# Kernel optimization log

Measured on AMD Instinct MI355X. Metric: run time of the kernel, lower is better.

Reference implementation:

```python
import jax, jax.numpy as jnp
import numpy as np

V, P, D, H, HD, L, FF = 21128, 512, 768, 12, 64, 12, 3072
COEF = np.array([[1,1,0,0,0,0,0,0,0,0,0,1],[1,1,1,1,0,0,0,0,0,0,0,1],[1,1,1,1,1,1,0,0,0,0,0,1],[1,1,1,1,1,1,1,1,0,0,0,1],[1,1,1,1,1,1,1,1,1,1,0,1]], dtype=np.float32)

def _ln(x, g, b):
    mu = jnp.mean(x, -1, keepdims=True)
    v = jnp.mean((x - mu) ** 2, -1, keepdims=True)
    return (x - mu) / jnp.sqrt(v + 1e-12) * g + b

def _gelu(x):
    return x * 0.5 * (1.0 + jax.lax.erf(x * 0.7071067811865475))

def setup_inputs() -> dict:
    key = jax.random.key(0)
    ks = jax.random.split(key, 16)
    B, S, LE = 16, 512, 256
    input_ids = jax.random.randint(ks[0], (B, S), 0, V)
    mask = jnp.ones((B, S), jnp.float32)
    epid = jax.random.randint(ks[1], (B, LE), 0, 10)
    epid = epid.at[:, -1].set(9)  # ensure encoder_turn=9 -> coefficient row 4
    s = 0.02
    def nrm(k, shape):
        return jax.random.normal(k, shape, jnp.float32) * s
    return {
        'input_ids': input_ids, 'mask': mask, 'encoder_position_id': epid,
        'word_emb': nrm(ks[2], (V, D)), 'pos_emb': nrm(ks[3], (P, D)),
        'emb_ln_g': jnp.ones((D,)), 'emb_ln_b': jnp.zeros((D,)),
        'Wq': nrm(ks[4], (L, D, D)), 'bq': jnp.zeros((L, D)),
        'Wk': nrm(ks[5], (L, D, D)), 'bk': jnp.zeros((L, D)),
        'Wv': nrm(ks[6], (L, D, D)), 'bv': jnp.zeros((L, D)),
        'Wo': nrm(ks[7], (L, D, D)), 'bo': jnp.zeros((L, D)),
        'ln1_g': jnp.ones((L, D)), 'ln1_b': jnp.zeros((L, D)),
        'Wi': nrm(ks[8], (L, D, FF)), 'bi': jnp.zeros((L, FF)),
        'Wo2': nrm(ks[9], (L, FF, D)), 'bo2': jnp.zeros((L, D)),
        'ln2_g': jnp.ones((L, D)), 'ln2_b': jnp.zeros((L, D)),
        'coef': jnp.tile(jnp.asarray(COEF)[None], (L, 1, 1)),
    }

def reference(input_ids, mask, encoder_position_id, word_emb, pos_emb, emb_ln_g, emb_ln_b,
              Wq, bq, Wk, bk, Wv, bv, Wo, bo, ln1_g, ln1_b, Wi, bi, Wo2, bo2, ln2_g, ln2_b, coef):
    B, S = input_ids.shape
    LE = encoder_position_id.shape[1]
    # causal+padding mask: floor((m+m^T)/2) on {0,1} == AND == product, then tril
    am = jnp.tril(mask[:, None, None, :] * mask[:, None, :, None])  # [B,1,S,S]
    # position coefficient machinery
    turn = jnp.max(encoder_position_id, -1)           # [B]
    row = ((turn - 1) // 2).astype(jnp.int32)         # row into [5,12] table
    enc_pm = jax.nn.one_hot(encoder_position_id, 12, dtype=jnp.float32)  # [B,LE,12]
    dec_pm = jnp.zeros((B, S - LE, 12), jnp.float32).at[:, :, 11].set(1.0)
    pm = jnp.concatenate([enc_pm, dec_pm], 1)         # [B,S,12]
    # embeddings (token_type not used in forward; past_length=0)
    h = _ln(word_emb[input_ids] + pos_emb[jnp.arange(S)], emb_ln_g, emb_ln_b)
    for l in range(L):
        coef_row = coef[l][row]                       # [B,12]
        ps = jnp.einsum('bsk,bk->bs', pm, coef_row)   # per-key modulation [B,S]
        q = (h @ Wq[l] + bq[l]).reshape(B, S, H, HD)
        k = (h @ Wk[l] + bk[l]).reshape(B, S, H, HD)
        v = (h @ Wv[l] + bv[l]).reshape(B, S, H, HD)
        scores = jnp.einsum('bqhd,bkhd->bhqk', q, k) / 8.0
        scores = scores * ps[:, None, None, :]
        scores = scores * am - 1e10 * (1.0 - am)
        probs = jax.nn.softmax(scores, -1)
        ctx = jnp.einsum('bhqk,bkhd->bqhd', probs, v).reshape(B, S, D)
        a = _ln(ctx @ Wo[l] + bo[l] + h, ln1_g[l], ln1_b[l])
        ff = _gelu(a @ Wi[l] + bi[l])
        h = _ln(ff @ Wo2[l] + bo2[l] + a, ln2_g[l], ln2_b[l])
    return h
```

## Files before the change

kernel.cpp:

```cpp
#include <hip/hip_runtime.h>

#define SEQ 512
#define NB  16
#define DIM 768
#define NH  12
#define HDIM 64
#define NL  12
#define FFD 3072
#define MTOK 8192
#define QKVD 2304

typedef _Float16 half8 __attribute__((ext_vector_type(8)));
typedef float    floatx4 __attribute__((ext_vector_type(4)));

__device__ __forceinline__ void load_lds16(const void* g, void* l) {
  __builtin_amdgcn_global_load_lds((__attribute__((address_space(1))) void*)g,
                                   (__attribute__((address_space(3))) void*)l, 16, 0, 0);
}

__device__ __forceinline__ float blockSum768(float v) {
  __shared__ float red[4];
  #pragma unroll
  for (int d = 32; d; d >>= 1) v += __shfl_xor(v, d);
  const int wv = threadIdx.x >> 6;
  __syncthreads();
  if ((threadIdx.x & 63) == 0) red[wv] = v;
  __syncthreads();
  return red[0] + red[1] + red[2] + red[3];
}

__device__ __forceinline__ void ln_store(float x0, float x1, float x2,
                                         const float* __restrict__ g,
                                         const float* __restrict__ bb,
                                         float* __restrict__ yf,
                                         _Float16* __restrict__ yh, int row) {
  const int tid = threadIdx.x;
  const float mu = blockSum768(x0 + x1 + x2) * (1.0f / 768.0f);
  const float d0 = x0 - mu, d1 = x1 - mu, d2 = x2 - mu;
  const float var = blockSum768(d0 * d0 + d1 * d1 + d2 * d2) * (1.0f / 768.0f);
  const float inv = rsqrtf(var + 1e-12f);
  const size_t base = (size_t)row * DIM;
  const float y0 = d0 * inv * g[tid]       + bb[tid];
  const float y1 = d1 * inv * g[tid + 256] + bb[tid + 256];
  const float y2 = d2 * inv * g[tid + 512] + bb[tid + 512];
  if (yf) { yf[base + tid] = y0; yf[base + tid + 256] = y1; yf[base + tid + 512] = y2; }
  yh[base + tid] = (_Float16)y0; yh[base + tid + 256] = (_Float16)y1; yh[base + tid + 512] = (_Float16)y2;
}

__global__ __launch_bounds__(256) void embed_ln_k(const int* __restrict__ ids,
                                                  const float* __restrict__ we,
                                                  const float* __restrict__ pe,
                                                  const float* __restrict__ g,
                                                  const float* __restrict__ bb,
                                                  float* __restrict__ hf,
                                                  _Float16* __restrict__ hh) {
  const int tok = blockIdx.x;
  const int s = tok & (SEQ - 1);
  const int id = ids[tok];
  const int tid = threadIdx.x;
  float x[3];
  #pragma unroll
  for (int j = 0; j < 3; ++j) {
    const int d = tid + j * 256;
    x[j] = we[(size_t)id * DIM + d] + pe[(size_t)s * DIM + d];
  }
  ln_store(x[0], x[1], x[2], g, bb, hf, hh, tok);
}

__global__ __launch_bounds__(256) void ln_k(const float* __restrict__ xin,
                                            const float* __restrict__ g,
                                            const float* __restrict__ bb,
                                            float* __restrict__ yf,
                                            _Float16* __restrict__ yh) {
  const int row = blockIdx.x;
  const int tid = threadIdx.x;
  float x[3];
  #pragma unroll
  for (int j = 0; j < 3; ++j) x[j] = xin[(size_t)row * DIM + tid + j * 256];
  ln_store(x[0], x[1], x[2], g, bb, yf, yh, row);
}

__global__ __launch_bounds__(256) void transpose_k(const float* __restrict__ in,
                                                   _Float16* __restrict__ out,
                                                   int K, int N, size_t ozs) {
  __shared__ float tile[32][33];
  const int z = blockIdx.z;
  in  += (size_t)z * K * N;
  out += (size_t)z * ozs;
  const int n0 = blockIdx.x * 32, k0 = blockIdx.y * 32;
  const int tx = threadIdx.x & 31, ty = threadIdx.x >> 5;
  #pragma unroll
  for (int i = 0; i < 32; i += 8) tile[ty + i][tx] = in[(size_t)(k0 + ty + i) * N + n0 + tx];
  __syncthreads();
  #pragma unroll
  for (int i = 0; i < 32; i += 8) out[(size_t)(n0 + ty + i) * K + k0 + tx] = (_Float16)tile[tx][ty + i];
}

__global__ __launch_bounds__(256) void concat_bias_k(const float* __restrict__ bq,
                                                     const float* __restrict__ bk,
                                                     const float* __restrict__ bv,
                                                     float* __restrict__ dst) {
  const int l = blockIdx.x;
  for (int j = threadIdx.x; j < DIM; j += 256) {
    dst[(size_t)l * QKVD + j]           = bq[l * DIM + j];
    dst[(size_t)l * QKVD + DIM + j]     = bk[l * DIM + j];
    dst[(size_t)l * QKVD + 2 * DIM + j] = bv[l * DIM + j];
  }
}

__global__ __launch_bounds__(512) void ps_k(const int* __restrict__ epid,
                                            const float* __restrict__ coef,
                                            float* __restrict__ ps_all) {
  __shared__ int red[8];
  const int b = blockIdx.x, tid = threadIdx.x;
  int e = (tid < 256) ? epid[b * 256 + tid] : 0;
  #pragma unroll
  for (int d = 32; d; d >>= 1) e = max(e, __shfl_xor(e, d));
  if ((tid & 63) == 0) red[tid >> 6] = e;
  __syncthreads();
  int turn = red[0];
  #pragma unroll
  for (int i = 1; i < 8; ++i) turn = max(turn, red[i]);
  int row = (turn - 1) >> 1;
  row = max(0, min(4, row));
  const int pe = (tid < 256) ? epid[b * 256 + tid] : 11;
  #pragma unroll
  for (int l = 0; l < NL; ++l)
    ps_all[((size_t)l * NB + b) * SEQ + tid] = coef[(l * 5 + row) * 12 + pe];
}

template <bool RES, bool GELU, bool WF, bool WH>
__global__ __launch_bounds__(256) void gemm_f16(const _Float16* __restrict__ A,
                                                const _Float16* __restrict__ Bt,
                                                const float* __restrict__ bias,
                                                const float* __restrict__ resid,
                                                float* __restrict__ outF,
                                                _Float16* __restrict__ outH,
                                                int M, int N, int K) {
  __shared__ __align__(16) _Float16 Als[128 * 32];
  __shared__ __align__(16) _Float16 Bls[128 * 32];
  const int tid = threadIdx.x, lane = tid & 63, wave = tid >> 6;
  const int bm0 = blockIdx.y * 128, bn0 = blockIdx.x * 128;
  const int lr = lane & 15, lk = lane >> 4;
  const int wm = (wave >> 1) * 64, wn = (wave & 1) * 64;
  floatx4 acc[4][4] = {};

  const int srow = lane >> 2;
  const int scol = (lane & 3) * 8;
  const _Float16* Ag = A  + (size_t)(bm0 + wave * 16 + srow) * K + scol;
  const _Float16* Bg = Bt + (size_t)(bn0 + wave * 16 + srow) * K + scol;
  _Float16* Al = &Als[wave * 16 * 32];
  _Float16* Bl = &Bls[wave * 16 * 32];
  const size_t rs64 = (size_t)64 * K;

  for (int kt = 0; kt < K; kt += 32) {
    load_lds16(Ag + kt,        Al);
    load_lds16(Ag + rs64 + kt, Al + 64 * 32);
    load_lds16(Bg + kt,        Bl);
    load_lds16(Bg + rs64 + kt, Bl + 64 * 32);
    __syncthreads();
    half8 af[4], bf[4];
    #pragma unroll
    for (int i = 0; i < 4; ++i) {
      af[i] = *(const half8*)&Als[(wm + i * 16 + lr) * 32 + lk * 8];
      bf[i] = *(const half8*)&Bls[(wn + i * 16 + lr) * 32 + lk * 8];
    }
    #pragma unroll
    for (int mi = 0; mi < 4; ++mi)
      #pragma unroll
      for (int ni = 0; ni < 4; ++ni)
        acc[mi][ni] = __builtin_amdgcn_mfma_f32_16x16x32_f16(af[mi], bf[ni], acc[mi][ni], 0, 0, 0);
    __syncthreads();
  }

  #pragma unroll
  for (int mi = 0; mi < 4; ++mi) {
    #pragma unroll
    for (int r = 0; r < 4; ++r) {
      const int row = bm0 + wm + mi * 16 + lk * 4 + r;
      const size_t ro = (size_t)row * N;
      #pragma unroll
      for (int ni = 0; ni < 4; ++ni) {
        const int col = bn0 + wn + ni * 16 + lr;
        float x = acc[mi][ni][r] + bias[col];
        if (RES)  x += resid[ro + col];
        if (GELU) x = 0.5f * x * (1.0f + erff(x * 0.70710678118654752f));
        if (WF) outF[ro + col] = x;
        if (WH) outH[ro + col] = (_Float16)x;
      }
    }
  }
}

__global__ __launch_bounds__(256) void attn_k(const _Float16* __restrict__ qkv,
                                              const float* __restrict__ ps,
                                              const float* __restrict__ mask,
                                              _Float16* __restrict__ ctx) {
  __shared__ __align__(16) _Float16 kls[64 * 64];
  __shared__ __align__(16) _Float16 vtls[64 * 64];
  __shared__ __align__(16) _Float16 pls[4][32 * 64];
  const int tid = threadIdx.x, lane = tid & 63, wave = tid >> 6;
  const int qt = 3 - blockIdx.x;
  const int h = blockIdx.y, b = blockIdx.z;
  const int lr = lane & 15, lk = lane >> 4;
  const int q0 = qt * 128 + wave * 32;

  half8 qf[2][2];
  #pragma unroll
  for (int mi = 0; mi < 2; ++mi)
    #pragma unroll
    for (int ks = 0; ks < 2; ++ks)
      qf[mi][ks] = *(const half8*)&qkv[(size_t)(b * SEQ + q0 + mi * 16 + lr) * QKVD + h * HDIM + ks * 32 + lk * 8];

  floatx4 o[2][4] = {};
  float m_run[2][4], l_run[2][4], mq[2][4];
  #pragma unroll
  for (int mi = 0; mi < 2; ++mi)
    #pragma unroll
    for (int r = 0; r < 4; ++r) {
      m_run[mi][r] = -3e38f; l_run[mi][r] = 0.f;
      mq[mi][r] = mask[b * SEQ + q0 + mi * 16 + lk * 4 + r];
    }

  const int swzA = (lr & 7) * 8;
  const int nt = 2 * (qt + 1);
  for (int t = 0; t < nt; ++t) {
    const int kb = t * 64;
    #pragma unroll
    for (int i = 0; i < 2; ++i) {
      const int idx = tid + i * 256;
      const int key = idx >> 3, c8 = (idx & 7) * 8;
      *(half8*)&kls[key * 64 + (c8 ^ ((key & 7) * 8))] =
          *(const half8*)&qkv[(size_t)(b * SEQ + kb + key) * QKVD + DIM + h * HDIM + c8];
      const int keyv = idx & 63, c8v = (idx >> 6) * 8;
      half8 vv = *(const half8*)&qkv[(size_t)(b * SEQ + kb + keyv) * QKVD + 2 * DIM + h * HDIM + c8v];
      #pragma unroll
      for (int j = 0; j < 8; ++j) {
        const int d = c8v + j;
        vtls[d * 64 + (keyv ^ ((d & 7) * 8))] = vv[j];
      }
    }
    __syncthreads();

    floatx4 s[2][4] = {};
    #pragma unroll
    for (int ks = 0; ks < 2; ++ks)
      #pragma unroll
      for (int ni = 0; ni < 4; ++ni) {
        half8 kf = *(const half8*)&kls[(ni * 16 + lr) * 64 + ((ks * 32 + lk * 8) ^ swzA)];
        #pragma unroll
        for (int mi = 0; mi < 2; ++mi)
          s[mi][ni] = __builtin_amdgcn_mfma_f32_16x16x32_f16(qf[mi][ks], kf, s[mi][ni], 0, 0, 0);
      }

    float pk[4], km[4]; int kidx[4];
    #pragma unroll
    for (int ni = 0; ni < 4; ++ni) {
      kidx[ni] = kb + ni * 16 + lr;
      pk[ni] = ps[b * SEQ + kidx[ni]] * 0.125f;
      km[ni] = mask[b * SEQ + kidx[ni]];
    }

    #pragma unroll
    for (int mi = 0; mi < 2; ++mi) {
      #pragma unroll
      for (int r = 0; r < 4; ++r) {
        const int rq = q0 + mi * 16 + lk * 4 + r;
        const int prow = mi * 16 + lk * 4 + r;
        const int pswz = (prow & 7) * 8;
        float sc[4]; float mt = -3e38f;
        #pragma unroll
        for (int ni = 0; ni < 4; ++ni) {
          const float am = (kidx[ni] <= rq) ? km[ni] * mq[mi][r] : 0.f;
          const float x = s[mi][ni][r] * pk[ni] * am - 1e10f * (1.f - am);
          sc[ni] = x; mt = fmaxf(mt, x);
        }
        #pragma unroll
        for (int d = 1; d < 16; d <<= 1) mt = fmaxf(mt, __shfl_xor(mt, d));
        const float mnew = fmaxf(m_run[mi][r], mt);
        const float corr = __expf(m_run[mi][r] - mnew);
        float rsum = 0.f;
        #pragma unroll
        for (int ni = 0; ni < 4; ++ni) {
          const float p = __expf(sc[ni] - mnew);
          rsum += p;
          pls[wave][prow * 64 + ((ni * 16 + lr) ^ pswz)] = (_Float16)p;
        }
        #pragma unroll
        for (int d = 1; d < 16; d <<= 1) rsum += __shfl_xor(rsum, d);
        l_run[mi][r] = l_run[mi][r] * corr + rsum;
        m_run[mi][r] = mnew;
        #pragma unroll
        for (int ni = 0; ni < 4; ++ni) o[mi][ni][r] *= corr;
      }
    }

    #pragma unroll
    for (int mi = 0; mi < 2; ++mi) {
      half8 pf[2];
      #pragma unroll
      for (int ks = 0; ks < 2; ++ks)
        pf[ks] = *(const half8*)&pls[wave][(mi * 16 + lr) * 64 + ((ks * 32 + lk * 8) ^ swzA)];
      #pragma unroll
      for (int ni = 0; ni < 4; ++ni)
        #pragma unroll
        for (int ks = 0; ks < 2; ++ks)
          o[mi][ni] = __builtin_amdgcn_mfma_f32_16x16x32_f16(
              pf[ks], *(const half8*)&vtls[(ni * 16 + lr) * 64 + ((ks * 32 + lk * 8) ^ swzA)], o[mi][ni], 0, 0, 0);
    }
    __syncthreads();
  }

  #pragma unroll
  for (int mi = 0; mi < 2; ++mi)
    #pragma unroll
    for (int r = 0; r < 4; ++r) {
      const float inv = 1.f / l_run[mi][r];
      const int rq = q0 + mi * 16 + lk * 4 + r;
      #pragma unroll
      for (int ni = 0; ni < 4; ++ni)
        ctx[(size_t)(b * SEQ + rq) * DIM + h * HDIM + ni * 16 + lr] = (_Float16)(o[mi][ni][r] * inv);
    }
}

extern "C" void kernel_launch(void* const* d_in, const int* in_sizes, int n_in,
                              void* d_out, int out_size, void* d_ws, size_t ws_size,
                              hipStream_t stream) {
  const int*   ids  = (const int*)d_in[0];
  const float* mask = (const float*)d_in[1];
  const int*   epid = (const int*)d_in[2];
  const float* we   = (const float*)d_in[3];
  const float* pe   = (const float*)d_in[4];
  const float* elng = (const float*)d_in[5];
  const float* elnb = (const float*)d_in[6];
  const float* Wq   = (const float*)d_in[7];  const float* bq  = (const float*)d_in[8];
  const float* Wk   = (const float*)d_in[9];  const float* bk  = (const float*)d_in[10];
  const float* Wv   = (const float*)d_in[11]; const float* bv  = (const float*)d_in[12];
  const float* Wo   = (const float*)d_in[13]; const float* bo  = (const float*)d_in[14];
  const float* ln1g = (const float*)d_in[15]; const float* ln1b = (const float*)d_in[16];
  const float* Wi   = (const float*)d_in[17]; const float* bi  = (const float*)d_in[18];
  const float* Wo2  = (const float*)d_in[19]; const float* bo2 = (const float*)d_in[20];
  const float* ln2g = (const float*)d_in[21]; const float* ln2b = (const float*)d_in[22];
  const float* coef = (const float*)d_in[23];
  float* out = (float*)d_out;

  char* w = (char*)d_ws;
  auto alloc = [&](size_t bytes) { char* p = w; w += (bytes + 255) & ~(size_t)255; return p; };
  const size_t WSM = (size_t)DIM * DIM;
  const size_t WLG = (size_t)DIM * FFD;
  _Float16* wqkvT = (_Float16*)alloc(NL * 3 * WSM * 2);
  _Float16* woT   = (_Float16*)alloc(NL * WSM * 2);
  _Float16* wiT   = (_Float16*)alloc(NL * WLG * 2);
  _Float16* wo2T  = (_Float16*)alloc(NL * WLG * 2);
  float*    bqkv  = (float*)alloc((size_t)NL * QKVD * 4);
  float*    h_f32 = (float*)alloc((size_t)MTOK * DIM * 4);
  _Float16* h_f16 = (_Float16*)alloc((size_t)MTOK * DIM * 2);
  float*    a_f32 = (float*)alloc((size_t)MTOK * DIM * 4);
  _Float16* a_f16 = (_Float16*)alloc((size_t)MTOK * DIM * 2);
  float*    tmp   = (float*)alloc((size_t)MTOK * DIM * 4);
  _Float16* qkv_f16 = (_Float16*)alloc((size_t)MTOK * QKVD * 2);
  _Float16* c_f16 = (_Float16*)alloc((size_t)MTOK * DIM * 2);
  _Float16* ff_f16 = (_Float16*)alloc((size_t)MTOK * FFD * 2);
  float*    ps_all = (float*)alloc((size_t)NL * NB * SEQ * 4);

  transpose_k<<<dim3(24, 24, NL), 256, 0, stream>>>(Wq, wqkvT,           DIM, DIM, 3 * WSM);
  transpose_k<<<dim3(24, 24, NL), 256, 0, stream>>>(Wk, wqkvT + WSM,     DIM, DIM, 3 * WSM);
  transpose_k<<<dim3(24, 24, NL), 256, 0, stream>>>(Wv, wqkvT + 2 * WSM, DIM, DIM, 3 * WSM);
  transpose_k<<<dim3(24, 24, NL), 256, 0, stream>>>(Wo,  woT,  DIM, DIM, WSM);
  transpose_k<<<dim3(96, 24, NL), 256, 0, stream>>>(Wi,  wiT,  DIM, FFD, WLG);
  transpose_k<<<dim3(24, 96, NL), 256, 0, stream>>>(Wo2, wo2T, FFD, DIM, WLG);
  concat_bias_k<<<NL, 256, 0, stream>>>(bq, bk, bv, bqkv);
  ps_k<<<NB, 512, 0, stream>>>(epid, coef, ps_all);
  embed_ln_k<<<MTOK, 256, 0, stream>>>(ids, we, pe, elng, elnb, h_f32, h_f16);

  for (int l = 0; l < NL; ++l) {
    gemm_f16<false, false, false, true><<<dim3(18, 64), 256, 0, stream>>>(
        h_f16, wqkvT + (size_t)l * 3 * WSM, bqkv + (size_t)l * QKVD, nullptr,
        nullptr, qkv_f16, MTOK, QKVD, DIM);
    attn_k<<<dim3(4, NH, NB), 256, 0, stream>>>(
        qkv_f16, ps_all + (size_t)l * NB * SEQ, mask, c_f16);
    gemm_f16<true, false, true, false><<<dim3(6, 64), 256, 0, stream>>>(
        c_f16, woT + (size_t)l * WSM, bo + l * DIM, h_f32, tmp, nullptr, MTOK, DIM, DIM);
    ln_k<<<MTOK, 256, 0, stream>>>(tmp, ln1g + l * DIM, ln1b + l * DIM, a_f32, a_f16);
    gemm_f16<false, true, false, true><<<dim3(24, 64), 256, 0, stream>>>(
        a_f16, wiT + (size_t)l * WLG, bi + l * FFD, nullptr, nullptr, ff_f16, MTOK, FFD, DIM);
    gemm_f16<true, false, true, false><<<dim3(6, 64), 256, 0, stream>>>(
        ff_f16, wo2T + (size_t)l * WLG, bo2 + l * DIM, a_f32, tmp, nullptr, MTOK, DIM, FFD);
    ln_k<<<MTOK, 256, 0, stream>>>(tmp, ln2g + l * DIM, ln2b + l * DIM,
                                   (l == NL - 1) ? out : h_f32, h_f16);
  }
}
```

Before: 4.658 ms.

## Double-buffer GEMM LDS tiles, swizzle workgroups, split-K the FFN down projection

The GEMM kernel now uses two LDS buffers so the next K-slice's global-to-LDS load is issued while the current slice is computed, with one barrier per slice instead of two. Workgroup indices are remapped in an XCD-aware pattern (grouped by blockIdx mod 8) over a 1D grid. The FFN down-projection (K=3072) is split into two K halves written to separate fp32 buffers, which the following layernorm sums, doubling the grid from 384 blocks to better fill the device. The cost is an extra fp32 intermediate write and read and doubled LDS use per block.

```diff
diff --git a/kernel.cpp b/kernel.cpp
--- a/kernel.cpp
+++ b/kernel.cpp
@@ -68,6 +68,7 @@
 }
 
 __global__ __launch_bounds__(256) void ln_k(const float* __restrict__ xin,
+                                            const float* __restrict__ xin2,
                                             const float* __restrict__ g,
                                             const float* __restrict__ bb,
                                             float* __restrict__ yf,
@@ -76,7 +77,10 @@
   const int tid = threadIdx.x;
   float x[3];
   #pragma unroll
-  for (int j = 0; j < 3; ++j) x[j] = xin[(size_t)row * DIM + tid + j * 256];
+  for (int j = 0; j < 3; ++j) {
+    const size_t idx = (size_t)row * DIM + tid + j * 256;
+    x[j] = xin[idx] + (xin2 ? xin2[idx] : 0.f);
+  }
   ln_store(x[0], x[1], x[2], g, bb, yf, yh, row);
 }
 
@@ -135,44 +139,70 @@
                                                 const float* __restrict__ bias,
                                                 const float* __restrict__ resid,
                                                 float* __restrict__ outF,
+                                                float* __restrict__ outF2,
                                                 _Float16* __restrict__ outH,
-                                                int M, int N, int K) {
-  __shared__ __align__(16) _Float16 Als[128 * 32];
-  __shared__ __align__(16) _Float16 Bls[128 * 32];
+                                                int N, int Kpart, int lda, int ldb,
+                                                int nbx, int nby) {
+  __shared__ __align__(16) _Float16 As0[128 * 32], Bs0[128 * 32];
+  __shared__ __align__(16) _Float16 As1[128 * 32], Bs1[128 * 32];
   const int tid = threadIdx.x, lane = tid & 63, wave = tid >> 6;
-  const int bm0 = blockIdx.y * 128, bn0 = blockIdx.x * 128;
+
+  const int chunk = gridDim.x >> 3;
+  int wg = blockIdx.x;
+  wg = (wg & 7) * chunk + (wg >> 3);
+  const int tiles = nbx * nby;
+  const int s = wg / tiles;
+  const int rem = wg - s * tiles;
+  const int bn0 = (rem % nbx) * 128;
+  const int bm0 = (rem / nbx) * 128;
+  const int koff = s * Kpart;
+
   const int lr = lane & 15, lk = lane >> 4;
   const int wm = (wave >> 1) * 64, wn = (wave & 1) * 64;
   floatx4 acc[4][4] = {};
 
   const int srow = lane >> 2;
   const int scol = (lane & 3) * 8;
-  const _Float16* Ag = A  + (size_t)(bm0 + wave * 16 + srow) * K + scol;
-  const _Float16* Bg = Bt + (size_t)(bn0 + wave * 16 + srow) * K + scol;
-  _Float16* Al = &Als[wave * 16 * 32];
-  _Float16* Bl = &Bls[wave * 16 * 32];
-  const size_t rs64 = (size_t)64 * K;
-
-  for (int kt = 0; kt < K; kt += 32) {
-    load_lds16(Ag + kt,        Al);
-    load_lds16(Ag + rs64 + kt, Al + 64 * 32);
-    load_lds16(Bg + kt,        Bl);
-    load_lds16(Bg + rs64 + kt, Bl + 64 * 32);
-    __syncthreads();
+  const _Float16* Ag = A  + (size_t)(bm0 + wave * 16 + srow) * lda + koff + scol;
+  const _Float16* Bg = Bt + (size_t)(bn0 + wave * 16 + srow) * ldb + koff + scol;
+  const size_t ars64 = (size_t)64 * lda;
+  const size_t brs64 = (size_t)64 * ldb;
+  const int wo = wave * 512;
+
+  auto STAGE = [&](_Float16* Ab, _Float16* Bb, int kt) {
+    const int o = kt * 32;
+    load_lds16(Ag + o,         Ab + wo);
+    load_lds16(Ag + ars64 + o, Ab + 2048 + wo);
+    load_lds16(Bg + o,         Bb + wo);
+    load_lds16(Bg + brs64 + o, Bb + 2048 + wo);
+  };
+  auto COMPUTE = [&](const _Float16* Ab, const _Float16* Bb) {
     half8 af[4], bf[4];
     #pragma unroll
     for (int i = 0; i < 4; ++i) {
-      af[i] = *(const half8*)&Als[(wm + i * 16 + lr) * 32 + lk * 8];
-      bf[i] = *(const half8*)&Bls[(wn + i * 16 + lr) * 32 + lk * 8];
+      af[i] = *(const half8*)&Ab[(wm + i * 16 + lr) * 32 + lk * 8];
+      bf[i] = *(const half8*)&Bb[(wn + i * 16 + lr) * 32 + lk * 8];
     }
     #pragma unroll
     for (int mi = 0; mi < 4; ++mi)
       #pragma unroll
       for (int ni = 0; ni < 4; ++ni)
         acc[mi][ni] = __builtin_amdgcn_mfma_f32_16x16x32_f16(af[mi], bf[ni], acc[mi][ni], 0, 0, 0);
+  };
+
+  const int nk = Kpart >> 5;
+  STAGE(As0, Bs0, 0);
+  __syncthreads();
+  for (int kt = 0; kt < nk; kt += 2) {
+    STAGE(As1, Bs1, kt + 1);
+    COMPUTE(As0, Bs0);
     __syncthreads();
-  }
-
+    if (kt + 2 < nk) STAGE(As0, Bs0, kt + 2);
+    COMPUTE(As1, Bs1);
+    __syncthreads();
+  }
+
+  const bool first = (s == 0);
   #pragma unroll
   for (int mi = 0; mi < 4; ++mi) {
     #pragma unroll
@@ -182,10 +212,11 @@
       #pragma unroll
       for (int ni = 0; ni < 4; ++ni) {
         const int col = bn0 + wn + ni * 16 + lr;
-        float x = acc[mi][ni][r] + bias[col];
-        if (RES)  x += resid[ro + col];
+        float x = acc[mi][ni][r];
+        if (first) x += bias[col];
+        if (RES)  if (first) x += resid[ro + col];
         if (GELU) x = 0.5f * x * (1.0f + erff(x * 0.70710678118654752f));
-        if (WF) outF[ro + col] = x;
+        if (WF) (first ? outF : outF2)[ro + col] = x;
         if (WH) outH[ro + col] = (_Float16)x;
       }
     }
@@ -358,6 +389,7 @@
   float*    a_f32 = (float*)alloc((size_t)MTOK * DIM * 4);
   _Float16* a_f16 = (_Float16*)alloc((size_t)MTOK * DIM * 2);
   float*    tmp   = (float*)alloc((size_t)MTOK * DIM * 4);
+  float*    tmp2  = (float*)alloc((size_t)MTOK * DIM * 4);
   _Float16* qkv_f16 = (_Float16*)alloc((size_t)MTOK * QKVD * 2);
   _Float16* c_f16 = (_Float16*)alloc((size_t)MTOK * DIM * 2);
   _Float16* ff_f16 = (_Float16*)alloc((size_t)MTOK * FFD * 2);
@@ -374,19 +406,22 @@
   embed_ln_k<<<MTOK, 256, 0, stream>>>(ids, we, pe, elng, elnb, h_f32, h_f16);
 
   for (int l = 0; l < NL; ++l) {
-    gemm_f16<false, false, false, true><<<dim3(18, 64), 256, 0, stream>>>(
+    gemm_f16<false, false, false, true><<<18 * 64, 256, 0, stream>>>(
         h_f16, wqkvT + (size_t)l * 3 * WSM, bqkv + (size_t)l * QKVD, nullptr,
-        nullptr, qkv_f16, MTOK, QKVD, DIM);
+        nullptr, nullptr, qkv_f16, QKVD, DIM, DIM, DIM, 18, 64);
     attn_k<<<dim3(4, NH, NB), 256, 0, stream>>>(
         qkv_f16, ps_all + (size_t)l * NB * SEQ, mask, c_f16);
-    gemm_f16<true, false, true, false><<<dim3(6, 64), 256, 0, stream>>>(
-        c_f16, woT + (size_t)l * WSM, bo + l * DIM, h_f32, tmp, nullptr, MTOK, DIM, DIM);
-    ln_k<<<MTOK, 256, 0, stream>>>(tmp, ln1g + l * DIM, ln1b + l * DIM, a_f32, a_f16);
-    gemm_f16<false, true, false, true><<<dim3(24, 64), 256, 0, stream>>>(
-        a_f16, wiT + (size_t)l * WLG, bi + l * FFD, nullptr, nullptr, ff_f16, MTOK, FFD, DIM);
-    gemm_f16<true, false, true, false><<<dim3(6, 64), 256, 0, stream>>>(
-        ff_f16, wo2T + (size_t)l * WLG, bo2 + l * DIM, a_f32, tmp, nullptr, MTOK, DIM, FFD);
-    ln_k<<<MTOK, 256, 0, stream>>>(tmp, ln2g + l * DIM, ln2b + l * DIM,
+    gemm_f16<true, false, true, false><<<6 * 64, 256, 0, stream>>>(
+        c_f16, woT + (size_t)l * WSM, bo + l * DIM, h_f32,
+        tmp, nullptr, nullptr, DIM, DIM, DIM, DIM, 6, 64);
+    ln_k<<<MTOK, 256, 0, stream>>>(tmp, nullptr, ln1g + l * DIM, ln1b + l * DIM, a_f32, a_f16);
+    gemm_f16<false, true, false, true><<<24 * 64, 256, 0, stream>>>(
+        a_f16, wiT + (size_t)l * WLG, bi + l * FFD, nullptr,
+        nullptr, nullptr, ff_f16, FFD, DIM, DIM, DIM, 24, 64);
+    gemm_f16<true, false, true, false><<<6 * 64 * 2, 256, 0, stream>>>(
+        ff_f16, wo2T + (size_t)l * WLG, bo2 + l * DIM, a_f32,
+        tmp, tmp2, nullptr, DIM, FFD / 2, FFD, FFD, 6, 64);
+    ln_k<<<MTOK, 256, 0, stream>>>(tmp, tmp2, ln2g + l * DIM, ln2b + l * DIM,
                                    (l == NL - 1) ? out : h_f32, h_f16);
   }
 }
```

Result: slower. 6.181 ms (+32.7%).
